# Performance work log

Measured on AMD Instinct MI355X. Metric: run time of the kernel, lower is better.

Reference implementation:

```python
import jax, jax.numpy as jnp
import numpy as np

RCUT = 6.0
RCUT_SMTH = 0.5


def _smooth_cosine(r):
    # piecewise: 1 for r < rcut_smth; 0.5*cos(pi*u)+0.5 for rcut_smth <= r < rcut; 0 beyond
    u = (r - RCUT_SMTH) / (RCUT - RCUT_SMTH)
    mid = 0.5 * jnp.cos(jnp.float32(np.pi) * u) + 0.5
    return jnp.where(r < RCUT_SMTH, jnp.ones_like(r),
                     jnp.where(r < RCUT, mid, jnp.zeros_like(r)))


def setup_inputs() -> dict:
    key = jax.random.key(0)
    k1, k2 = jax.random.split(key)
    B, F, N = 4, 4, 1024
    coord = jax.random.normal(k1, (B, F, N, 3), dtype=jnp.float32) * 5.0
    atype = jax.random.randint(k2, (B, N), 0, 2, dtype=jnp.int64)
    return {"coord": coord, "atype": atype}


def reference(coord, atype):
    # coord: [B, F, N, 3] -> descriptor [B, F, N*3]
    B, F, N, _ = coord.shape
    # pairwise difference: diff[b,f,i,j,:] = coord[b,f,i] - coord[b,f,j]
    diff = coord[:, :, :, None, :] - coord[:, :, None, :, :]  # [B,F,N,N,3]
    dist = jnp.sqrt(jnp.sum(diff * diff, axis=-1) + 1e-10)     # [B,F,N,N]
    s_ij = _smooth_cosine(dist)                                # [B,F,N,N]
    desc = jnp.sum(s_ij[..., None] * diff, axis=3)             # [B,F,N,3]
    return desc.reshape(B, F, N * 3)
```

## Files before the change

kernel.cpp:

```cpp
#include <hip/hip_runtime.h>


#define NA   1024
#define IPB  16
#define JLEN 64

__global__ __launch_bounds__(256) void desc_kernel(const float* __restrict__ coord,
                                                   float* __restrict__ out) {
    __shared__ float4 s_c[NA];
    __shared__ float  s_red[4][IPB][3];

    const int tid     = threadIdx.x;
    const int blk     = blockIdx.x;
    const int frame   = blk >> 6;
    const int ibk     = blk & 63;
    const int i_local = tid & 15;
    const int jc      = tid >> 4;

    const float* gf = coord + frame * (NA * 3);

    for (int a = tid; a < NA; a += 256) {
        s_c[a] = make_float4(gf[3 * a], gf[3 * a + 1], gf[3 * a + 2], 0.0f);
    }
    __syncthreads();

    const int    i  = ibk * IPB + i_local;
    const float4 ci = s_c[i];
    const float  cx = ci.x, cy = ci.y, cz = ci.z;

    float ax = 0.0f, ay = 0.0f, az = 0.0f;
    const int   jbase = jc * JLEN;
    const float INV11 = 1.0f / 11.0f;
    const float OFF   = -0.5f / 11.0f;

#pragma unroll 8
    for (int t = 0; t < JLEN; ++t) {
        const int    j  = jbase + ((t + jc) & (JLEN - 1));
        const float4 cj = s_c[j];
        const float  dx = cx - cj.x;
        const float  dy = cy - cj.y;
        const float  dz = cz - cj.z;
        const float  d2 = fmaf(dx, dx, fmaf(dy, dy, fmaf(dz, dz, 1e-10f)));
        const float  r  = __builtin_amdgcn_sqrtf(d2);
        float rev = fmaf(r, INV11, OFF);
        rev = fminf(fmaxf(rev, 0.0f), 0.5f);
        const float s = fmaf(0.5f, __builtin_amdgcn_cosf(rev), 0.5f);
        ax = fmaf(s, dx, ax);
        ay = fmaf(s, dy, ay);
        az = fmaf(s, dz, az);
    }

    ax += __shfl_xor(ax, 16, 64); ax += __shfl_xor(ax, 32, 64);
    ay += __shfl_xor(ay, 16, 64); ay += __shfl_xor(ay, 32, 64);
    az += __shfl_xor(az, 16, 64); az += __shfl_xor(az, 32, 64);

    const int wave = tid >> 6;
    if ((tid & 48) == 0) {
        s_red[wave][i_local][0] = ax;
        s_red[wave][i_local][1] = ay;
        s_red[wave][i_local][2] = az;
    }
    __syncthreads();

    if (tid < IPB * 3) {
        const int il   = tid / 3;
        const int comp = tid - il * 3;
        const float v = s_red[0][il][comp] + s_red[1][il][comp] +
                        s_red[2][il][comp] + s_red[3][il][comp];
        out[frame * (NA * 3) + (ibk * IPB + il) * 3 + comp] = v;
    }
}

extern "C" void kernel_launch(void* const* d_in, const int* in_sizes, int n_in,
                              void* d_out, int out_size, void* d_ws, size_t ws_size,
                              hipStream_t stream) {
    const float* coord = (const float*)d_in[0];
    float*       out   = (float*)d_out;
    (void)d_ws; (void)ws_size; (void)n_in; (void)out_size;

    const int frames = in_sizes[0] / (NA * 3);
    const int blocks = frames * (NA / IPB);

    hipLaunchKernelGGL(desc_kernel, dim3(blocks), dim3(256), 0, stream, coord, out);
}
```

Before: 63.40 us.

## Register-block four i-atoms per thread and pad shared coords

```diff
diff --git a/kernel.cpp b/kernel.cpp
--- a/kernel.cpp
+++ b/kernel.cpp
@@ -1,72 +1,88 @@
 #include <hip/hip_runtime.h>
 
 
-#define NA   1024
-#define IPB  16
-#define JLEN 64
+#define NA     1024
+#define IPB    32
+#define IPT    4
+#define JLEN   32
+#define STRIDE 33
 
 __global__ __launch_bounds__(256) void desc_kernel(const float* __restrict__ coord,
                                                    float* __restrict__ out) {
-    __shared__ float4 s_c[NA];
-    __shared__ float  s_red[4][IPB][3];
+    __shared__ float4 s_c[32 * STRIDE];
+    __shared__ float  s_red[4][8][IPT][3];
 
-    const int tid     = threadIdx.x;
-    const int blk     = blockIdx.x;
-    const int frame   = blk >> 6;
-    const int ibk     = blk & 63;
-    const int i_local = tid & 15;
-    const int jc      = tid >> 4;
+    const int tid   = threadIdx.x;
+    const int blk   = blockIdx.x;
+    const int frame = blk >> 5;
+    const int ibk   = blk & 31;
+    const int ig    = tid & 7;
+    const int jc    = tid >> 3;
 
     const float* gf = coord + frame * (NA * 3);
 
     for (int a = tid; a < NA; a += 256) {
-        s_c[a] = make_float4(gf[3 * a], gf[3 * a + 1], gf[3 * a + 2], 0.0f);
+        const int slot = (a >> 5) * STRIDE + (a & 31);
+        s_c[slot] = make_float4(gf[3 * a], gf[3 * a + 1], gf[3 * a + 2], 0.0f);
     }
     __syncthreads();
 
-    const int    i  = ibk * IPB + i_local;
-    const float4 ci = s_c[i];
-    const float  cx = ci.x, cy = ci.y, cz = ci.z;
+    float cx[IPT], cy[IPT], cz[IPT];
+    float ax[IPT], ay[IPT], az[IPT];
+#pragma unroll
+    for (int k = 0; k < IPT; ++k) {
+        const float4 c = s_c[ibk * STRIDE + ig * IPT + k];
+        cx[k] = c.x; cy[k] = c.y; cz[k] = c.z;
+        ax[k] = 0.0f; ay[k] = 0.0f; az[k] = 0.0f;
+    }
 
-    float ax = 0.0f, ay = 0.0f, az = 0.0f;
-    const int   jbase = jc * JLEN;
     const float INV11 = 1.0f / 11.0f;
     const float OFF   = -0.5f / 11.0f;
+    const float4* cb = &s_c[jc * STRIDE];
 
-#pragma unroll 8
+#pragma unroll 4
     for (int t = 0; t < JLEN; ++t) {
-        const int    j  = jbase + ((t + jc) & (JLEN - 1));
-        const float4 cj = s_c[j];
-        const float  dx = cx - cj.x;
-        const float  dy = cy - cj.y;
-        const float  dz = cz - cj.z;
-        const float  d2 = fmaf(dx, dx, fmaf(dy, dy, fmaf(dz, dz, 1e-10f)));
-        const float  r  = __builtin_amdgcn_sqrtf(d2);
-        float rev = fmaf(r, INV11, OFF);
-        rev = fminf(fmaxf(rev, 0.0f), 0.5f);
-        const float s = fmaf(0.5f, __builtin_amdgcn_cosf(rev), 0.5f);
-        ax = fmaf(s, dx, ax);
-        ay = fmaf(s, dy, ay);
-        az = fmaf(s, dz, az);
+        const float4 cj = cb[t];
+#pragma unroll
+        for (int k = 0; k < IPT; ++k) {
+            const float dx = cx[k] - cj.x;
+            const float dy = cy[k] - cj.y;
+            const float dz = cz[k] - cj.z;
+            const float d2 = fmaf(dx, dx, fmaf(dy, dy, fmaf(dz, dz, 1e-10f)));
+            const float r  = __builtin_amdgcn_sqrtf(d2);
+            const float rev = __builtin_amdgcn_fmed3f(fmaf(r, INV11, OFF), 0.0f, 0.5f);
+            const float s  = fmaf(0.5f, __builtin_amdgcn_cosf(rev), 0.5f);
+            ax[k] = fmaf(s, dx, ax[k]);
+            ay[k] = fmaf(s, dy, ay[k]);
+            az[k] = fmaf(s, dz, az[k]);
+        }
     }
 
-    ax += __shfl_xor(ax, 16, 64); ax += __shfl_xor(ax, 32, 64);
-    ay += __shfl_xor(ay, 16, 64); ay += __shfl_xor(ay, 32, 64);
-    az += __shfl_xor(az, 16, 64); az += __shfl_xor(az, 32, 64);
+#pragma unroll
+    for (int k = 0; k < IPT; ++k) {
+        ax[k] += __shfl_xor(ax[k], 8, 64);  ax[k] += __shfl_xor(ax[k], 16, 64);  ax[k] += __shfl_xor(ax[k], 32, 64);
+        ay[k] += __shfl_xor(ay[k], 8, 64);  ay[k] += __shfl_xor(ay[k], 16, 64);  ay[k] += __shfl_xor(ay[k], 32, 64);
+        az[k] += __shfl_xor(az[k], 8, 64);  az[k] += __shfl_xor(az[k], 16, 64);  az[k] += __shfl_xor(az[k], 32, 64);
+    }
 
     const int wave = tid >> 6;
-    if ((tid & 48) == 0) {
-        s_red[wave][i_local][0] = ax;
-        s_red[wave][i_local][1] = ay;
-        s_red[wave][i_local][2] = az;
+    if ((tid & 56) == 0) {
+#pragma unroll
+        for (int k = 0; k < IPT; ++k) {
+            s_red[wave][ig][k][0] = ax[k];
+            s_red[wave][ig][k][1] = ay[k];
+            s_red[wave][ig][k][2] = az[k];
+        }
     }
     __syncthreads();
 
     if (tid < IPB * 3) {
         const int il   = tid / 3;
         const int comp = tid - il * 3;
-        const float v = s_red[0][il][comp] + s_red[1][il][comp] +
-                        s_red[2][il][comp] + s_red[3][il][comp];
+        const int g    = il >> 2;
+        const int k    = il & 3;
+        const float v = s_red[0][g][k][comp] + s_red[1][g][k][comp] +
+                        s_red[2][g][k][comp] + s_red[3][g][k][comp];
         out[frame * (NA * 3) + (ibk * IPB + il) * 3 + comp] = v;
     }
 }
```

Result: no change. 63.48 us (+0.1%).
